# Kernel tuning notes

Hardware: AMD Instinct MI355X
Metric: run time of the kernel (lower is better)

## Reference

```python
import jax, jax.numpy as jnp
import numpy as np

N = 100000      # num POIs (nodes)
M = 20000       # num trajectories (hyperedges)
NNZ = 1000000   # incidence entries
D = 128         # emb_dim
NUM_LAYERS = 3
NEG_SLOPE = 0.2  # PyG HypergraphConv leaky_relu default


def setup_inputs() -> dict:
    key = jax.random.key(0)
    ks = jax.random.split(key, 8)
    pois_embs = jax.random.normal(ks[0], (N, D), jnp.float32)
    traj_embs = jax.random.normal(ks[1], (M, D), jnp.float32)
    hyperedge_weight = jax.random.uniform(ks[2], (M,), jnp.float32)
    node_idx = jax.random.randint(ks[3], (NNZ,), 0, N, jnp.int32)
    edge_idx = jax.random.randint(ks[4], (NNZ,), 0, M, jnp.int32)
    # learned params of the shared HypergraphConv layer (heads=1, concat)
    W_lin = jax.random.normal(ks[5], (D, D), jnp.float32) / np.sqrt(D).astype(np.float32)
    att = jax.random.normal(ks[6], (2 * D,), jnp.float32) * 0.1
    bias = jnp.zeros((D,), jnp.float32)
    return dict(pois_embs=pois_embs, traj_embs=traj_embs,
                hyperedge_weight=hyperedge_weight,
                node_idx=node_idx, edge_idx=edge_idx,
                W_lin=W_lin, att=att, bias=bias)


def _segment_softmax(scores, seg, num_seg):
    smax = jax.ops.segment_max(scores, seg, num_segments=num_seg)
    smax = jnp.where(jnp.isfinite(smax), smax, 0.0)  # guard empty segments
    ex = jnp.exp(scores - smax[seg])
    den = jax.ops.segment_sum(ex, seg, num_segments=num_seg)
    return ex / (den[seg] + 1e-16)


def _hconv(x, traj_embs, hyperedge_weight, node_idx, edge_idx, W_lin, att, bias):
    # x: [N, D] node feats; traj_embs: [M, D] hyperedge feats
    xt = x @ W_lin            # [N, D]  lin(x)
    et = traj_embs @ W_lin    # [M, D]  lin(hyperedge_attr)
    # attention logits per incidence pair (additive decomposition of cat*att)
    s_n = xt @ att[:D]        # [N]
    s_e = et @ att[D:]        # [M]
    alpha = jax.nn.leaky_relu(s_n[node_idx] + s_e[edge_idx], NEG_SLOPE)  # [NNZ]
    alpha = _segment_softmax(alpha, node_idx, N)  # softmax grouped by node
    # degree normalizations: D = sum_e H_ve * w_e, B = |e|
    Ddeg = jax.ops.segment_sum(hyperedge_weight[edge_idx], node_idx, num_segments=N)
    Dinv = jnp.where(Ddeg > 0, 1.0 / Ddeg, 0.0)
    Bdeg = jax.ops.segment_sum(jnp.ones((NNZ,), xt.dtype), edge_idx, num_segments=M)
    Binv = jnp.where(Bdeg > 0, 1.0 / Bdeg, 0.0)
    # node -> edge: B^{-1} H^T (alpha * x)
    msg1 = (alpha * Binv[edge_idx])[:, None] * xt[node_idx]        # [NNZ, D]
    edge_out = jax.ops.segment_sum(msg1, edge_idx, num_segments=M)  # [M, D]
    # edge -> node: D^{-1} H (alpha * edge_out)
    msg2 = (alpha * Dinv[node_idx])[:, None] * edge_out[edge_idx]   # [NNZ, D]
    out = jax.ops.segment_sum(msg2, node_idx, num_segments=N)       # [N, D]
    return out + bias


def reference(pois_embs, traj_embs, hyperedge_weight, node_idx, edge_idx, W_lin, att, bias):
    cur = pois_embs
    acc = pois_embs  # running sum of stacked layer outputs (incl. input)
    for _ in range(NUM_LAYERS):
        cur = _hconv(cur, traj_embs, hyperedge_weight, node_idx, edge_idx, W_lin, att, bias) + cur
        acc = acc + cur
    return acc / jnp.asarray(NUM_LAYERS + 1, acc.dtype)  # mean over stack
```

## Files before the change

### kernel.cpp

```cpp
#include <hip/hip_runtime.h>
#include <hip/hip_fp16.h>
#include <cstdint>
#include <cstddef>
#include <cstring>

#define DIM 128
#define NEG_SLOPE 0.2f

#define EREP 16
#define NREP 8

typedef _Float16 half8v __attribute__((ext_vector_type(8)));
typedef __attribute__((ext_vector_type(4))) float float4v;

__device__ __forceinline__ float2 h2f2(uint u) {
  __half2 h;
  __builtin_memcpy(&h, &u, 4);
  return __half22float2(h);
}
__device__ __forceinline__ uint packh2(float lo, float hi) {
  __half2 h = __floats2half2_rn(lo, hi);
  uint u;
  __builtin_memcpy(&u, &h, 4);
  return u;
}
__device__ __forceinline__ ushort f2h_us(float f) {
  __half h = __float2half_rn(f);
  ushort us;
  __builtin_memcpy(&us, &h, 2);
  return us;
}
__device__ __forceinline__ float lrelu(float x) {
  return x >= 0.0f ? x : NEG_SLOPE * x;
}

__global__ void wswz_kernel(const float* __restrict__ W, ushort* __restrict__ Wswz)
{
  int i = blockIdx.x * 256 + threadIdx.x;
  int j = i & 7, lane = (i >> 3) & 63, nt = (i >> 9) & 7, kt = i >> 12;
  int k = kt * 32 + (lane >> 4) * 8 + j;
  int col = nt * 16 + (lane & 15);
  Wswz[i] = f2h_us(W[k * 128 + col]);
}

__global__ void poish_kernel(const float* __restrict__ pois,
                             uint4* __restrict__ pois_h, int N_, int NP)
{
  int i = blockIdx.x * 256 + threadIdx.x;
  if (i >= NP * 16) return;
  int row = i >> 4;
  uint4 o;
  if (row < N_) {
    const float* src = pois + (size_t)i * 8;
    float4 f0 = *(const float4*)src;
    float4 f1 = *(const float4*)(src + 4);
    o.x = packh2(f0.x, f0.y); o.y = packh2(f0.z, f0.w);
    o.z = packh2(f1.x, f1.y); o.w = packh2(f1.z, f1.w);
  } else { o.x = o.y = o.z = o.w = 0; }
  pois_h[i] = o;
}

__global__ __launch_bounds__(256) void gemm_mfma_kernel(
    const ushort* __restrict__ Xb, const ushort* __restrict__ Wswz,
    const float* __restrict__ att, ushort* __restrict__ Yb,
    float* __restrict__ s_n, int rowsN)
{
  __shared__ ushort st[64 * 128];
  int tid = threadIdx.x;
  int w = tid >> 6, lane = tid & 63;
  int q = lane >> 4, c = lane & 15;
  int r0b = blockIdx.x * 64;
  int r0 = r0b + w * 16;
  float4v acc[8];
#pragma unroll
  for (int nt = 0; nt < 8; ++nt) acc[nt] = (float4v){0.f, 0.f, 0.f, 0.f};
  const ushort* arow = Xb + (size_t)(r0 + c) * DIM + q * 8;
#pragma unroll
  for (int kt = 0; kt < 4; ++kt) {
    half8v a = *(const half8v*)(arow + kt * 32);
#pragma unroll
    for (int nt = 0; nt < 8; ++nt) {
      half8v b = *(const half8v*)(Wswz + ((((kt << 3) + nt) << 9) + (lane << 3)));
      acc[nt] = __builtin_amdgcn_mfma_f32_16x16x32_f16(a, b, acc[nt], 0, 0, 0);
    }
  }
  float av[8];
#pragma unroll
  for (int nt = 0; nt < 8; ++nt) av[nt] = att[nt * 16 + c];
  float p0 = 0, p1 = 0, p2 = 0, p3 = 0;
#pragma unroll
  for (int nt = 0; nt < 8; ++nt) {
    p0 = fmaf(acc[nt][0], av[nt], p0);
    p1 = fmaf(acc[nt][1], av[nt], p1);
    p2 = fmaf(acc[nt][2], av[nt], p2);
    p3 = fmaf(acc[nt][3], av[nt], p3);
  }
#pragma unroll
  for (int m = 8; m >= 1; m >>= 1) {
    p0 += __shfl_xor(p0, m, 64);
    p1 += __shfl_xor(p1, m, 64);
    p2 += __shfl_xor(p2, m, 64);
    p3 += __shfl_xor(p3, m, 64);
  }
  if (c == 0) {
    int rb = r0 + q * 4;
    if (rb + 0 < rowsN) s_n[rb + 0] = p0;
    if (rb + 1 < rowsN) s_n[rb + 1] = p1;
    if (rb + 2 < rowsN) s_n[rb + 2] = p2;
    if (rb + 3 < rowsN) s_n[rb + 3] = p3;
  }
  ushort* sw = st + w * 2048;
#pragma unroll
  for (int nt = 0; nt < 8; ++nt) {
    sw[(q * 4 + 0) * 128 + nt * 16 + c] = f2h_us(acc[nt][0]);
    sw[(q * 4 + 1) * 128 + nt * 16 + c] = f2h_us(acc[nt][1]);
    sw[(q * 4 + 2) * 128 + nt * 16 + c] = f2h_us(acc[nt][2]);
    sw[(q * 4 + 3) * 128 + nt * 16 + c] = f2h_us(acc[nt][3]);
  }
  __syncthreads();
#pragma unroll
  for (int it = 0; it < 4; ++it) {
    int idx = tid + it * 256;
    int row = idx >> 4, seg = idx & 15;
    *(uint4*)(Yb + (size_t)(r0b + row) * DIM + seg * 8) =
        *(const uint4*)&st[row * 128 + seg * 8];
  }
}

__global__ __launch_bounds__(256) void se_kernel(
    const float* __restrict__ traj, const float* __restrict__ W,
    const float* __restrict__ att, const float* __restrict__ hw,
    float* __restrict__ s_e, float2* __restrict__ se_hw, int M_)
{
  __shared__ float wv[128];
  int tid = threadIdx.x;
  if (tid < 128) {
    const float* wr = W + (size_t)tid * 128;
    float acc = 0.0f;
#pragma unroll 4
    for (int k = 0; k < 128; ++k) acc = fmaf(wr[k], att[DIM + k], acc);
    wv[tid] = acc;
  }
  __syncthreads();
  int e = blockIdx.x * 4 + (tid >> 6);
  int lane = tid & 63;
  if (e >= M_) return;
  const float* row = traj + (size_t)e * DIM;
  float v = row[lane] * wv[lane] + row[lane + 64] * wv[lane + 64];
#pragma unroll
  for (int d = 32; d > 0; d >>= 1) v += __shfl_down(v, d, 64);
  if (lane == 0) {
    s_e[e] = v;
    float2 g; g.x = v; g.y = hw[e];
    se_hw[e] = g;
  }
}

__global__ void hist_rank_kernel(const int* __restrict__ node_idx,
                                 const int* __restrict__ edge_idx,
                                 int* __restrict__ ncnt_r, int* __restrict__ ecnt_r,
                                 int* __restrict__ r_n, int* __restrict__ r_e,
                                 int nnz, int M_, int N_)
{
  int t = blockIdx.x * blockDim.x + threadIdx.x;
  int j = t * 2;
  if (j >= nnz) return;
  int* ec = ecnt_r + (size_t)(t & (EREP - 1)) * M_;
  int* nc = ncnt_r + (size_t)(t & (NREP - 1)) * N_;
  if (j + 2 <= nnz) {
    int2 e = *(const int2*)&edge_idx[j];
    int2 n = *(const int2*)&node_idx[j];
    int a0 = atomicAdd(&ec[e.x], 1);
    int a1 = atomicAdd(&ec[e.y], 1);
    int b0 = atomicAdd(&nc[n.x], 1);
    int b1 = atomicAdd(&nc[n.y], 1);
    *(int2*)&r_e[j] = make_int2(a0, a1);
    *(int2*)&r_n[j] = make_int2(b0, b1);
  } else {
    r_e[j] = atomicAdd(&ec[edge_idx[j]], 1);
    r_n[j] = atomicAdd(&nc[node_idx[j]], 1);
  }
}

__global__ void repsum_kernel(int* __restrict__ cnt_r, int* __restrict__ cnt,
                              int nbins, int reps)
{
  int b = blockIdx.x * blockDim.x + threadIdx.x;
  if (b >= nbins) return;
  int s = 0;
  for (int r = 0; r < reps; ++r) {
    size_t o = (size_t)r * nbins + b;
    int v = cnt_r[o];
    cnt_r[o] = s;
    s += v;
  }
  cnt[b] = s;
}

__global__ __launch_bounds__(1024) void scan_block_kernel(
    const int* __restrict__ cnt, int* __restrict__ off,
    int* __restrict__ partials, int nbins)
{
  __shared__ int ws[16];
  int tid = threadIdx.x, lane = tid & 63, wid = tid >> 6;
  int base = blockIdx.x * 4096 + tid * 4;
  int x0 = base + 0 < nbins ? cnt[base + 0] : 0;
  int x1 = base + 1 < nbins ? cnt[base + 1] : 0;
  int x2 = base + 2 < nbins ? cnt[base + 2] : 0;
  int x3 = base + 3 < nbins ? cnt[base + 3] : 0;
  int t = x0 + x1 + x2 + x3;
  int v = t;
#pragma unroll
  for (int d = 1; d < 64; d <<= 1) {
    int y = __shfl_up(v, d, 64);
    if (lane >= d) v += y;
  }
  if (lane == 63) ws[wid] = v;
  __syncthreads();
  if (tid < 16) {
    int s = ws[tid];
#pragma unroll
    for (int d = 1; d < 16; d <<= 1) {
      int y = __shfl_up(s, d, 16);
      if (tid >= d) s += y;
    }
    ws[tid] = s;
  }
  __syncthreads();
  int pre = (wid > 0 ? ws[wid - 1] : 0) + (v - t);
  if (base + 0 < nbins) off[base + 0] = pre;
  if (base + 1 < nbins) off[base + 1] = pre + x0;
  if (base + 2 < nbins) off[base + 2] = pre + x0 + x1;
  if (base + 3 < nbins) off[base + 3] = pre + x0 + x1 + x2;
  if (tid == 0) partials[blockIdx.x] = ws[15];
}

__global__ __launch_bounds__(64) void scan_partials_kernel(
    int* __restrict__ partials, int nb)
{
  int lane = threadIdx.x;
  int t = lane < nb ? partials[lane] : 0;
  int v = t;
#pragma unroll
  for (int d = 1; d < 64; d <<= 1) {
    int y = __shfl_up(v, d, 64);
    if (lane >= d) v += y;
  }
  if (lane < nb) partials[lane] = v - t;
  if (lane == 63) partials[nb] = v;
}

__global__ void add_off_combine_kernel(int* __restrict__ off,
                                       const int* __restrict__ partials,
                                       int* __restrict__ pre,
                                       int nbins, int nb, int reps)
{
  int i = blockIdx.x * blockDim.x + threadIdx.x;
  if (i < nbins) {
    int o = off[i] + partials[i >> 12];
    off[i] = o;
    for (int r = 0; r < reps; ++r) pre[(size_t)r * nbins + i] += o;
  }
  if (i == 0) off[nbins] = partials[nb];
}

__global__ void scatter_edge_kernel(const int* __restrict__ node_idx,
                                    const int* __restrict__ edge_idx,
                                    const int* __restrict__ r_e,
                                    const int* __restrict__ pre_e,
                                    int* __restrict__ nd_e, int nnz, int M_)
{
  int j = (blockIdx.x * blockDim.x + threadIdx.x) * 4;
  if (j >= nnz) return;
  if (j + 4 <= nnz) {
    const int* p0 = pre_e + (size_t)((j >> 1) & (EREP - 1)) * M_;
    const int* p1 = pre_e + (size_t)(((j >> 1) + 1) & (EREP - 1)) * M_;
    int4 e = *(const int4*)&edge_idx[j];
    int4 n = *(const int4*)&node_idx[j];
    int4 re = *(const int4*)&r_e[j];
    nd_e[p0[e.x] + re.x] = n.x;
    nd_e[p0[e.y] + re.y] = n.y;
    nd_e[p1[e.z] + re.z] = n.z;
    nd_e[p1[e.w] + re.w] = n.w;
  } else {
    for (int k = j; k < nnz; ++k) {
      const int* pp = pre_e + (size_t)((k >> 1) & (EREP - 1)) * M_;
      nd_e[pp[edge_idx[k]] + r_e[k]] = node_idx[k];
    }
  }
}

__global__ void scatter_node_kernel(const int* __restrict__ node_idx,
                                    const int* __restrict__ edge_idx,
                                    const int* __restrict__ r_n,
                                    const int* __restrict__ pre_n,
                                    int* __restrict__ eidx_n, int nnz, int N_)
{
  int j = (blockIdx.x * blockDim.x + threadIdx.x) * 4;
  if (j >= nnz) return;
  if (j + 4 <= nnz) {
    const int* p0 = pre_n + (size_t)((j >> 1) & (NREP - 1)) * N_;
    const int* p1 = pre_n + (size_t)(((j >> 1) + 1) & (NREP - 1)) * N_;
    int4 e = *(const int4*)&edge_idx[j];
    int4 n = *(const int4*)&node_idx[j];
    int4 rn = *(const int4*)&r_n[j];
    eidx_n[p0[n.x] + rn.x] = e.x;
    eidx_n[p0[n.y] + rn.y] = e.y;
    eidx_n[p1[n.z] + rn.z] = e.z;
    eidx_n[p1[n.w] + rn.w] = e.w;
  } else {
    for (int k = j; k < nnz; ++k) {
      const int* pp = pre_n + (size_t)((k >> 1) & (NREP - 1)) * N_;
      eidx_n[pp[node_idx[k]] + r_n[k]] = edge_idx[k];
    }
  }
}

__global__ void softstat_kernel(const int* __restrict__ noff,
                                const int* __restrict__ eidx_n,
                                const float* __restrict__ s_n,
                                const float2* __restrict__ se_hw,
                                float2* __restrict__ ns2,
                                float* __restrict__ Dinv, int N_)
{
  int n = blockIdx.x * blockDim.x + threadIdx.x;
  if (n >= N_) return;
  int s = noff[n], e1 = noff[n + 1];
  float sn = s_n[n];
  float m = -INFINITY, den = 0.0f, d = 0.0f;
  int t = s;
  for (; t + 4 <= e1; t += 4) {
    int i0 = eidx_n[t], i1 = eidx_n[t + 1], i2 = eidx_n[t + 2], i3 = eidx_n[t + 3];
    float2 g0 = se_hw[i0], g1 = se_hw[i1], g2 = se_hw[i2], g3 = se_hw[i3];
    float l0 = lrelu(sn + g0.x), l1 = lrelu(sn + g1.x);
    float l2 = lrelu(sn + g2.x), l3 = lrelu(sn + g3.x);
    float mm = fmaxf(fmaxf(fmaxf(l0, l1), fmaxf(l2, l3)), m);
    den = den * __expf(m - mm) + __expf(l0 - mm) + __expf(l1 - mm)
        + __expf(l2 - mm) + __expf(l3 - mm);
    m = mm;
    d += g0.y + g1.y + g2.y + g3.y;
  }
  for (; t < e1; ++t) {
    float2 g = se_hw[eidx_n[t]];
    float l = lrelu(sn + g.x);
    float mm = fmaxf(l, m);
    den = den * __expf(m - mm) + __expf(l - mm);
    m = mm;
    d += g.y;
  }
  if (s == e1) m = 0.0f;
  float2 r;
  r.x = sn;
  r.y = m + __logf(den + 1e-16f);
  ns2[n] = r;
  Dinv[n] = d > 0.0f ? 1.0f / d : 0.0f;
}

__global__ __launch_bounds__(256) void msg1_kernel(
    const int* __restrict__ eoff, const int* __restrict__ nd_e,
    const float2* __restrict__ ns2, const float* __restrict__ s_e,
    const uint4* __restrict__ xt16, uint4* __restrict__ eo16, int M_)
{
  int e = blockIdx.x * 4 + (threadIdx.x >> 6);
  int lane = threadIdx.x & 63;
  int r = lane >> 4, c = lane & 15;
  if (e >= M_) return;
  int s = eoff[e], t1 = eoff[e + 1];
  int len = t1 - s;
  float binv = len > 0 ? 1.0f / (float)len : 0.0f;
  float se = s_e[e];
  float acc[8];
#pragma unroll
  for (int j = 0; j < 8; ++j) acc[j] = 0.0f;
  for (int t = s; t < t1; t += 8) {
#pragma unroll
    for (int h = 0; h < 2; ++h) {
      int tb = t + h * 4;
      if (tb < t1) {
        int ti = tb + r;
        int tc = ti < t1 ? ti : t1 - 1;
        float valid = ti < t1 ? 1.0f : 0.0f;
        int nd = nd_e[tc];
        float2 q = ns2[nd];
        float coef = valid * __expf(lrelu(q.x + se) - q.y);
        uint4 g = xt16[(size_t)nd * 16 + c];
        float2 f0 = h2f2(g.x), f1 = h2f2(g.y), f2 = h2f2(g.z), f3 = h2f2(g.w);
        acc[0] = fmaf(coef, f0.x, acc[0]);
        acc[1] = fmaf(coef, f0.y, acc[1]);
        acc[2] = fmaf(coef, f1.x, acc[2]);
        acc[3] = fmaf(coef, f1.y, acc[3]);
        acc[4] = fmaf(coef, f2.x, acc[4]);
        acc[5] = fmaf(coef, f2.y, acc[5]);
        acc[6] = fmaf(coef, f3.x, acc[6]);
        acc[7] = fmaf(coef, f3.y, acc[7]);
      }
    }
  }
#pragma unroll
  for (int j = 0; j < 8; ++j) {
    acc[j] += __shfl_xor(acc[j], 16, 64);
    acc[j] += __shfl_xor(acc[j], 32, 64);
  }
  if (r == 0) {
    uint4 o;
    o.x = packh2(acc[0] * binv, acc[1] * binv);
    o.y = packh2(acc[2] * binv, acc[3] * binv);
    o.z = packh2(acc[4] * binv, acc[5] * binv);
    o.w = packh2(acc[6] * binv, acc[7] * binv);
    eo16[(size_t)e * 16 + c] = o;
  }
}

__global__ __launch_bounds__(256) void msg2_kernel(
    const int* __restrict__ noff, const int* __restrict__ eidx_n,
    const float2* __restrict__ ns2, const float* __restrict__ Dinv,
    const float* __restrict__ s_e, const uint4* __restrict__ eo16,
    const float* __restrict__ bias,
    const float* __restrict__ cin_f, const uint4* __restrict__ cin_h16,
    const float* __restrict__ x1f, const uint4* __restrict__ x2h16,
    uint4* __restrict__ couth16, float* __restrict__ dout,
    int mode, int N_)
{
  int n = blockIdx.x * 4 + (threadIdx.x >> 6);
  int lane = threadIdx.x & 63;
  int r = lane >> 4, c = lane & 15;
  if (n >= N_) return;
  int s = noff[n], t1 = noff[n + 1];
  float2 nsv = ns2[n];
  float sn = nsv.x, lz = nsv.y;
  float acc[8];
#pragma unroll
  for (int j = 0; j < 8; ++j) acc[j] = 0.0f;
  for (int t = s; t < t1; t += 8) {
#pragma unroll
    for (int h = 0; h < 2; ++h) {
      int tb = t + h * 4;
      if (tb < t1) {
        int ti = tb + r;
        int tc = ti < t1 ? ti : t1 - 1;
        float valid = ti < t1 ? 1.0f : 0.0f;
        int ed = eidx_n[tc];
        float xs = s_e[ed];
        float coef = valid * __expf(lrelu(sn + xs) - lz);
        uint4 g = eo16[(size_t)ed * 16 + c];
        float2 f0 = h2f2(g.x), f1 = h2f2(g.y), f2 = h2f2(g.z), f3 = h2f2(g.w);
        acc[0] = fmaf(coef, f0.x, acc[0]);
        acc[1] = fmaf(coef, f0.y, acc[1]);
        acc[2] = fmaf(coef, f1.x, acc[2]);
        acc[3] = fmaf(coef, f1.y, acc[3]);
        acc[4] = fmaf(coef, f2.x, acc[4]);
        acc[5] = fmaf(coef, f2.y, acc[5]);
        acc[6] = fmaf(coef, f3.x, acc[6]);
        acc[7] = fmaf(coef, f3.y, acc[7]);
      }
    }
  }
#pragma unroll
  for (int j = 0; j < 8; ++j) {
    acc[j] += __shfl_xor(acc[j], 16, 64);
    acc[j] += __shfl_xor(acc[j], 32, 64);
  }
  if (r != 0) return;
  float sc = Dinv[n];
  float cin[8];
  if (mode == 0) {
    const float4* cf = (const float4*)(cin_f + (size_t)n * DIM);
    float4 a = cf[c * 2], b = cf[c * 2 + 1];
    cin[0] = a.x; cin[1] = a.y; cin[2] = a.z; cin[3] = a.w;
    cin[4] = b.x; cin[5] = b.y; cin[6] = b.z; cin[7] = b.w;
  } else {
    uint4 ch = cin_h16[(size_t)n * 16 + c];
    float2 p0 = h2f2(ch.x), p1 = h2f2(ch.y), p2 = h2f2(ch.z), p3 = h2f2(ch.w);
    cin[0] = p0.x; cin[1] = p0.y; cin[2] = p1.x; cin[3] = p1.y;
    cin[4] = p2.x; cin[5] = p2.y; cin[6] = p3.x; cin[7] = p3.y;
  }
  const float4* bf = (const float4*)bias;
  float4 ba = bf[c * 2], bb = bf[c * 2 + 1];
  float bs[8] = {ba.x, ba.y, ba.z, ba.w, bb.x, bb.y, bb.z, bb.w};
  float cx[8];
#pragma unroll
  for (int j = 0; j < 8; ++j) cx[j] = cin[j] + acc[j] * sc + bs[j];
  if (mode == 2) {
    const float4* x1 = (const float4*)(x1f + (size_t)n * DIM);
    float4 xa = x1[c * 2], xb = x1[c * 2 + 1];
    float x1v[8] = {xa.x, xa.y, xa.z, xa.w, xb.x, xb.y, xb.z, xb.w};
    uint4 x2 = x2h16[(size_t)n * 16 + c];
    float2 y0 = h2f2(x2.x), y1 = h2f2(x2.y), y2 = h2f2(x2.z), y3 = h2f2(x2.w);
    float x2v[8] = {y0.x, y0.y, y1.x, y1.y, y2.x, y2.y, y3.x, y3.y};
    float4 o0, o1;
    o0.x = (x1v[0] + x2v[0] + cin[0] + cx[0]) * 0.25f;
    o0.y = (x1v[1] + x2v[1] + cin[1] + cx[1]) * 0.25f;
    o0.z = (x1v[2] + x2v[2] + cin[2] + cx[2]) * 0.25f;
    o0.w = (x1v[3] + x2v[3] + cin[3] + cx[3]) * 0.25f;
    o1.x = (x1v[4] + x2v[4] + cin[4] + cx[4]) * 0.25f;
    o1.y = (x1v[5] + x2v[5] + cin[5] + cx[5]) * 0.25f;
    o1.z = (x1v[6] + x2v[6] + cin[6] + cx[6]) * 0.25f;
    o1.w = (x1v[7] + x2v[7] + cin[7] + cx[7]) * 0.25f;
    float4* dp = (float4*)(dout + (size_t)n * DIM);
    dp[c * 2] = o0;
    dp[c * 2 + 1] = o1;
  } else {
    uint4 o;
    o.x = packh2(cx[0], cx[1]);
    o.y = packh2(cx[2], cx[3]);
    o.z = packh2(cx[4], cx[5]);
    o.w = packh2(cx[6], cx[7]);
    couth16[(size_t)n * 16 + c] = o;
  }
}

static inline int cdiv(int a, int b) { return (a + b - 1) / b; }

extern "C" void kernel_launch(void* const* d_in, const int* in_sizes, int n_in,
                              void* d_out, int out_size, void* d_ws, size_t ws_size,
                              hipStream_t stream)
{
  const float* pois = (const float*)d_in[0];
  const float* traj = (const float*)d_in[1];
  const float* hw   = (const float*)d_in[2];
  const int* node_idx = (const int*)d_in[3];
  const int* edge_idx = (const int*)d_in[4];
  const float* W    = (const float*)d_in[5];
  const float* att  = (const float*)d_in[6];
  const float* bias = (const float*)d_in[7];
  float* dout = (float*)d_out;

  const int N   = in_sizes[0] / DIM;
  const int M   = in_sizes[2];
  const int NNZ = in_sizes[3];
  const int NP  = (N + 63) & ~63;

  char* p = (char*)d_ws;
  auto alloc = [&](size_t bytes) -> void* {
    void* r = (void*)p;
    p += (bytes + 255) & ~(size_t)255;
    return r;
  };
  ushort* xt_h    = (ushort*)alloc((size_t)NP * DIM * 2);
  ushort* pois_h  = (ushort*)alloc((size_t)NP * DIM * 2);
  uint*   cura_h  = (uint*)alloc((size_t)NP * 64 * 4);
  uint*   curb_h  = (uint*)alloc((size_t)NP * 64 * 4);
  ushort* W_swz   = (ushort*)alloc(16384 * 2);
  uint*   eo_h  = (uint*)alloc((size_t)M * (DIM / 2) * 4);
  float2* ns2   = (float2*)alloc((size_t)N * 8);
  float*  s_e  = (float*)alloc((size_t)M * 4);
  float2* se_hw = (float2*)alloc((size_t)M * 8);
  float*  s_n  = (float*)alloc((size_t)N * 4);
  float*  Dinv = (float*)alloc((size_t)N * 4);
  int* ecnt   = (int*)alloc((size_t)M * 4);
  int* ncnt   = (int*)alloc((size_t)N * 4);
  int* ecnt_r = (int*)alloc((size_t)EREP * M * 4);
  int* ncnt_r = (int*)alloc((size_t)NREP * N * 4);
  int* eoff = (int*)alloc((size_t)(M + 1) * 4);
  int* noff = (int*)alloc((size_t)(N + 1) * 4);
  int* r_e  = (int*)alloc((size_t)NNZ * 4);
  int* r_n  = (int*)alloc((size_t)NNZ * 4);
  int* nd_e   = (int*)alloc((size_t)NNZ * 4);
  int* eidx_n = (int*)alloc((size_t)NNZ * 4);
  int* part_e = (int*)alloc(65 * 4);
  int* part_n = (int*)alloc(65 * 4);
  (void)ws_size;

  const int nbE = cdiv(M, 4096), nbN = cdiv(N, 4096);

  hipMemsetAsync(ecnt_r, 0, (size_t)EREP * M * 4, stream);
  hipMemsetAsync(ncnt_r, 0, (size_t)NREP * N * 4, stream);
  hist_rank_kernel<<<cdiv(NNZ, 512), 256, 0, stream>>>(node_idx, edge_idx, ncnt_r, ecnt_r, r_n, r_e, NNZ, M, N);
  repsum_kernel<<<cdiv(M, 256), 256, 0, stream>>>(ecnt_r, ecnt, M, EREP);
  repsum_kernel<<<cdiv(N, 256), 256, 0, stream>>>(ncnt_r, ncnt, N, NREP);
  scan_block_kernel<<<nbE, 1024, 0, stream>>>(ecnt, eoff, part_e, M);
  scan_block_kernel<<<nbN, 1024, 0, stream>>>(ncnt, noff, part_n, N);
  scan_partials_kernel<<<1, 64, 0, stream>>>(part_e, nbE);
  scan_partials_kernel<<<1, 64, 0, stream>>>(part_n, nbN);
  add_off_combine_kernel<<<cdiv(M, 256), 256, 0, stream>>>(eoff, part_e, ecnt_r, M, nbE, EREP);
  add_off_combine_kernel<<<cdiv(N, 256), 256, 0, stream>>>(noff, part_n, ncnt_r, N, nbN, NREP);
  scatter_edge_kernel<<<cdiv(NNZ, 1024), 256, 0, stream>>>(node_idx, edge_idx, r_e, ecnt_r, nd_e, NNZ, M);
  scatter_node_kernel<<<cdiv(NNZ, 1024), 256, 0, stream>>>(node_idx, edge_idx, r_n, ncnt_r, eidx_n, NNZ, N);

  wswz_kernel<<<64, 256, 0, stream>>>(W, W_swz);
  se_kernel<<<cdiv(M, 4), 256, 0, stream>>>(traj, W, att, hw, s_e, se_hw, M);
  poish_kernel<<<cdiv(NP * 16, 256), 256, 0, stream>>>(pois, (uint4*)pois_h, N, NP);

  for (int layer = 0; layer < 3; ++layer) {
    const ushort* gin = (layer == 0) ? pois_h
                       : (layer == 1) ? (const ushort*)cura_h
                                      : (const ushort*)curb_h;
    gemm_mfma_kernel<<<NP / 64, 256, 0, stream>>>(gin, W_swz, att, xt_h, s_n, N);
    softstat_kernel<<<cdiv(N, 256), 256, 0, stream>>>(noff, eidx_n, s_n, se_hw, ns2, Dinv, N);
    msg1_kernel<<<cdiv(M, 4), 256, 0, stream>>>(eoff, nd_e, ns2, s_e,
                                                (const uint4*)xt_h, (uint4*)eo_h, M);
    const uint* cin_h = (layer == 1) ? cura_h : curb_h;
    uint* couth = (layer == 0) ? cura_h : curb_h;
    msg2_kernel<<<cdiv(N, 4), 256, 0, stream>>>(noff, eidx_n, ns2, Dinv, s_e,
                                                (const uint4*)eo_h, bias,
                                                pois, (const uint4*)cin_h,
                                                pois, (const uint4*)cura_h,
                                                (uint4*)couth, dout, layer, N);
  }
}
```

Before: 691.4 us.

## Replace global-atomic replicated histograms with chunked LDS histograms for CSR build

Replaces the global-atomic histogram and rank computation, which used a few replicated count arrays, with per-chunk LDS histograms split into sub-bin ranges via a 2D grid. Each block counts one contiguous chunk of indices for one 16K-bin range in shared memory and writes per-chunk counts, which then feed the existing repsum/scan/scatter pipeline. The scatter kernels now look up the prefix by chunk index. This removes contended global atomics and the memsets, at the cost of each block re-reading its index chunk once per bin range and much larger per-chunk count arrays (about 123 chunks for edges, 31 for nodes) that the repsum and add-offset kernels must walk.

```diff
diff --git a/kernel.cpp b/kernel.cpp
--- a/kernel.cpp
+++ b/kernel.cpp
@@ -7,8 +7,9 @@
 #define DIM 128
 #define NEG_SLOPE 0.2f
 
-#define EREP 16
-#define NREP 8
+#define CHUNK_E_LOG 13
+#define CHUNK_N_LOG 15
+#define SUBBINS 16384
 
 typedef _Float16 half8v __attribute__((ext_vector_type(8)));
 typedef __attribute__((ext_vector_type(4))) float float4v;
@@ -156,30 +157,26 @@
   }
 }
 
-__global__ void hist_rank_kernel(const int* __restrict__ node_idx,
-                                 const int* __restrict__ edge_idx,
-                                 int* __restrict__ ncnt_r, int* __restrict__ ecnt_r,
-                                 int* __restrict__ r_n, int* __restrict__ r_e,
-                                 int nnz, int M_, int N_)
-{
-  int t = blockIdx.x * blockDim.x + threadIdx.x;
-  int j = t * 2;
-  if (j >= nnz) return;
-  int* ec = ecnt_r + (size_t)(t & (EREP - 1)) * M_;
-  int* nc = ncnt_r + (size_t)(t & (NREP - 1)) * N_;
-  if (j + 2 <= nnz) {
-    int2 e = *(const int2*)&edge_idx[j];
-    int2 n = *(const int2*)&node_idx[j];
-    int a0 = atomicAdd(&ec[e.x], 1);
-    int a1 = atomicAdd(&ec[e.y], 1);
-    int b0 = atomicAdd(&nc[n.x], 1);
-    int b1 = atomicAdd(&nc[n.y], 1);
-    *(int2*)&r_e[j] = make_int2(a0, a1);
-    *(int2*)&r_n[j] = make_int2(b0, b1);
-  } else {
-    r_e[j] = atomicAdd(&ec[edge_idx[j]], 1);
-    r_n[j] = atomicAdd(&nc[node_idx[j]], 1);
-  }
+__global__ __launch_bounds__(256) void hist_lds_kernel(
+    const int* __restrict__ idx, int* __restrict__ cnt_r,
+    int* __restrict__ rank, int nnz, int nbins, int chunk_log)
+{
+  __shared__ int h[SUBBINS];
+  int t0 = blockIdx.x << chunk_log;
+  int t1 = t0 + (1 << chunk_log);
+  if (t1 > nnz) t1 = nnz;
+  int base = blockIdx.y * SUBBINS;
+  int hi = base + SUBBINS;
+  if (hi > nbins) hi = nbins;
+  for (int i = threadIdx.x; i < SUBBINS; i += 256) h[i] = 0;
+  __syncthreads();
+  for (int j = t0 + threadIdx.x; j < t1; j += 256) {
+    int v = idx[j];
+    if (v >= base && v < hi) rank[j] = atomicAdd(&h[v - base], 1);
+  }
+  __syncthreads();
+  for (int i = base + threadIdx.x; i < hi; i += 256)
+    cnt_r[(size_t)blockIdx.x * nbins + i] = h[i - base];
 }
 
 __global__ void repsum_kernel(int* __restrict__ cnt_r, int* __restrict__ cnt,
@@ -273,18 +270,17 @@
   int j = (blockIdx.x * blockDim.x + threadIdx.x) * 4;
   if (j >= nnz) return;
   if (j + 4 <= nnz) {
-    const int* p0 = pre_e + (size_t)((j >> 1) & (EREP - 1)) * M_;
-    const int* p1 = pre_e + (size_t)(((j >> 1) + 1) & (EREP - 1)) * M_;
+    const int* pp = pre_e + (size_t)(j >> CHUNK_E_LOG) * M_;
     int4 e = *(const int4*)&edge_idx[j];
     int4 n = *(const int4*)&node_idx[j];
     int4 re = *(const int4*)&r_e[j];
-    nd_e[p0[e.x] + re.x] = n.x;
-    nd_e[p0[e.y] + re.y] = n.y;
-    nd_e[p1[e.z] + re.z] = n.z;
-    nd_e[p1[e.w] + re.w] = n.w;
+    nd_e[pp[e.x] + re.x] = n.x;
+    nd_e[pp[e.y] + re.y] = n.y;
+    nd_e[pp[e.z] + re.z] = n.z;
+    nd_e[pp[e.w] + re.w] = n.w;
   } else {
     for (int k = j; k < nnz; ++k) {
-      const int* pp = pre_e + (size_t)((k >> 1) & (EREP - 1)) * M_;
+      const int* pp = pre_e + (size_t)(k >> CHUNK_E_LOG) * M_;
       nd_e[pp[edge_idx[k]] + r_e[k]] = node_idx[k];
     }
   }
@@ -299,18 +295,17 @@
   int j = (blockIdx.x * blockDim.x + threadIdx.x) * 4;
   if (j >= nnz) return;
   if (j + 4 <= nnz) {
-    const int* p0 = pre_n + (size_t)((j >> 1) & (NREP - 1)) * N_;
-    const int* p1 = pre_n + (size_t)(((j >> 1) + 1) & (NREP - 1)) * N_;
+    const int* pp = pre_n + (size_t)(j >> CHUNK_N_LOG) * N_;
     int4 e = *(const int4*)&edge_idx[j];
     int4 n = *(const int4*)&node_idx[j];
     int4 rn = *(const int4*)&r_n[j];
-    eidx_n[p0[n.x] + rn.x] = e.x;
-    eidx_n[p0[n.y] + rn.y] = e.y;
-    eidx_n[p1[n.z] + rn.z] = e.z;
-    eidx_n[p1[n.w] + rn.w] = e.w;
+    eidx_n[pp[n.x] + rn.x] = e.x;
+    eidx_n[pp[n.y] + rn.y] = e.y;
+    eidx_n[pp[n.z] + rn.z] = e.z;
+    eidx_n[pp[n.w] + rn.w] = e.w;
   } else {
     for (int k = j; k < nnz; ++k) {
-      const int* pp = pre_n + (size_t)((k >> 1) & (NREP - 1)) * N_;
+      const int* pp = pre_n + (size_t)(k >> CHUNK_N_LOG) * N_;
       eidx_n[pp[node_idx[k]] + r_n[k]] = edge_idx[k];
     }
   }
@@ -529,6 +524,8 @@
   const int M   = in_sizes[2];
   const int NNZ = in_sizes[3];
   const int NP  = (N + 63) & ~63;
+  const int NBE = cdiv(NNZ, 1 << CHUNK_E_LOG);
+  const int NBN = cdiv(NNZ, 1 << CHUNK_N_LOG);
 
   char* p = (char*)d_ws;
   auto alloc = [&](size_t bytes) -> void* {
@@ -549,8 +546,8 @@
   float*  Dinv = (float*)alloc((size_t)N * 4);
   int* ecnt   = (int*)alloc((size_t)M * 4);
   int* ncnt   = (int*)alloc((size_t)N * 4);
-  int* ecnt_r = (int*)alloc((size_t)EREP * M * 4);
-  int* ncnt_r = (int*)alloc((size_t)NREP * N * 4);
+  int* ecnt_r = (int*)alloc((size_t)NBE * M * 4);
+  int* ncnt_r = (int*)alloc((size_t)NBN * N * 4);
   int* eoff = (int*)alloc((size_t)(M + 1) * 4);
   int* noff = (int*)alloc((size_t)(N + 1) * 4);
   int* r_e  = (int*)alloc((size_t)NNZ * 4);
@@ -563,17 +560,18 @@
 
   const int nbE = cdiv(M, 4096), nbN = cdiv(N, 4096);
 
-  hipMemsetAsync(ecnt_r, 0, (size_t)EREP * M * 4, stream);
-  hipMemsetAsync(ncnt_r, 0, (size_t)NREP * N * 4, stream);
-  hist_rank_kernel<<<cdiv(NNZ, 512), 256, 0, stream>>>(node_idx, edge_idx, ncnt_r, ecnt_r, r_n, r_e, NNZ, M, N);
-  repsum_kernel<<<cdiv(M, 256), 256, 0, stream>>>(ecnt_r, ecnt, M, EREP);
-  repsum_kernel<<<cdiv(N, 256), 256, 0, stream>>>(ncnt_r, ncnt, N, NREP);
+  hist_lds_kernel<<<dim3(NBE, cdiv(M, SUBBINS)), 256, 0, stream>>>(
+      edge_idx, ecnt_r, r_e, NNZ, M, CHUNK_E_LOG);
+  hist_lds_kernel<<<dim3(NBN, cdiv(N, SUBBINS)), 256, 0, stream>>>(
+      node_idx, ncnt_r, r_n, NNZ, N, CHUNK_N_LOG);
+  repsum_kernel<<<cdiv(M, 256), 256, 0, stream>>>(ecnt_r, ecnt, M, NBE);
+  repsum_kernel<<<cdiv(N, 256), 256, 0, stream>>>(ncnt_r, ncnt, N, NBN);
   scan_block_kernel<<<nbE, 1024, 0, stream>>>(ecnt, eoff, part_e, M);
   scan_block_kernel<<<nbN, 1024, 0, stream>>>(ncnt, noff, part_n, N);
   scan_partials_kernel<<<1, 64, 0, stream>>>(part_e, nbE);
   scan_partials_kernel<<<1, 64, 0, stream>>>(part_n, nbN);
-  add_off_combine_kernel<<<cdiv(M, 256), 256, 0, stream>>>(eoff, part_e, ecnt_r, M, nbE, EREP);
-  add_off_combine_kernel<<<cdiv(N, 256), 256, 0, stream>>>(noff, part_n, ncnt_r, N, nbN, NREP);
+  add_off_combine_kernel<<<cdiv(M, 256), 256, 0, stream>>>(eoff, part_e, ecnt_r, M, nbE, NBE);
+  add_off_combine_kernel<<<cdiv(N, 256), 256, 0, stream>>>(noff, part_n, ncnt_r, N, nbN, NBN);
   scatter_edge_kernel<<<cdiv(NNZ, 1024), 256, 0, stream>>>(node_idx, edge_idx, r_e, ecnt_r, nd_e, NNZ, M);
   scatter_node_kernel<<<cdiv(NNZ, 1024), 256, 0, stream>>>(node_idx, edge_idx, r_n, ncnt_r, eidx_n, NNZ, N);
 
```

New measurement: 755.0 us. 9.2% more time.
